# Performance work log

Hardware: AMD Instinct MI355X
Metric: run time of the kernel (lower is better)

Reference implementation:

```python
import jax, jax.numpy as jnp
import numpy as np

N_NODES = 50000
N_EDGES = 600000
D = 128


def setup_inputs() -> dict:
    key = jax.random.key(0)
    k1, k2, k3, k4, k5, k6 = jax.random.split(key, 6)
    x = jax.random.normal(k1, (N_NODES, D), dtype=jnp.float32)
    edge_index = jax.random.randint(k2, (2, N_EDGES), 0, N_NODES, dtype=jnp.int64)
    # nn.Linear default init: U(-1/sqrt(fan_in), 1/sqrt(fan_in))
    bound = 1.0 / np.sqrt(D)
    W1 = jax.random.uniform(k3, (D, D), minval=-bound, maxval=bound, dtype=jnp.float32)
    b1 = jax.random.uniform(k4, (D,), minval=-bound, maxval=bound, dtype=jnp.float32)
    W2 = jax.random.uniform(k5, (D, D), minval=-bound, maxval=bound, dtype=jnp.float32)
    b2 = jax.random.uniform(k6, (D,), minval=-bound, maxval=bound, dtype=jnp.float32)
    return {"x": x, "edge_index": edge_index, "W1": W1, "b1": b1, "W2": W2, "b2": b2}


def reference(x, edge_index, W1, b1, W2, b2):
    row, col = edge_index[0], edge_index[1]
    n = x.shape[0]
    # degree of each node as aggregation target, clamped to >= 1
    deg = jax.ops.segment_sum(jnp.ones(row.shape, dtype=x.dtype), row, num_segments=n)
    deg = jnp.maximum(deg, 1.0)[:, None]  # [N, 1]
    # round 1: gather neighbors, scatter-add by row, normalize, linear+relu
    agg = jax.ops.segment_sum(x[col], row, num_segments=n)  # [N, D]
    h = jax.nn.relu((agg / deg) @ W1.T + b1)
    # round 2
    agg2 = jax.ops.segment_sum(h[col], row, num_segments=n)  # [N, D]
    return jax.nn.relu((agg2 / deg) @ W2.T + b2)
```

## Files before the change

### kernel.cpp

```cpp
#include <hip/hip_runtime.h>
#include <hip/hip_fp16.h>

#define D 128
#define TILE_R 64
#define NC 8

typedef _Float16 h8 __attribute__((ext_vector_type(8)));
typedef float f4 __attribute__((ext_vector_type(4)));

__global__ __launch_bounds__(256) void prep_kernel(int* __restrict__ hist8, int n8,
                                                   const float* __restrict__ W1,
                                                   __half* __restrict__ WB1,
                                                   const float* __restrict__ W2,
                                                   __half* __restrict__ WB2) {
    if (blockIdx.x < 2) {
        const float* W = blockIdx.x ? W2 : W1;
        __half* WB     = blockIdx.x ? WB2 : WB1;
        for (int idx = threadIdx.x; idx < D * D; idx += 256) {
            int j  = idx & 7;
            int l  = (idx >> 3) & 63;
            int kk = (idx >> 9) & 3;
            int c  = idx >> 11;
            int k   = kk * 32 + (l >> 4) * 8 + j;
            int col = c * 16 + (l & 15);
            WB[idx] = __float2half(W[col * D + k]);
        }
        return;
    }
    int i = (blockIdx.x - 2) * 256 + threadIdx.x;
    if (i < n8) hist8[i] = 0;
}

__device__ inline h8 load_frag(const __half* p) { return *(const h8*)p; }
__device__ inline h8 load_frag(const float* p) {
    float4 u = *(const float4*)p;
    float4 v = *(const float4*)(p + 4);
    h8 r;
    r[0] = (_Float16)u.x; r[1] = (_Float16)u.y; r[2] = (_Float16)u.z; r[3] = (_Float16)u.w;
    r[4] = (_Float16)v.x; r[5] = (_Float16)v.y; r[6] = (_Float16)v.z; r[7] = (_Float16)v.w;
    return r;
}

template <typename T>
__device__ inline void linear_coal(const T* __restrict__ src,
                                   const __half* __restrict__ WB,
                                   __half* __restrict__ z, int n, int blk) {
    __shared__ __half Zs[64][132];
    int l    = threadIdx.x & 63;
    int wv   = threadIdx.x >> 6;
    int row0 = blk * TILE_R + wv * 16;
    int arow = row0 + (l & 15);
    bool rowok = arow < n;

    h8 a[4];
#pragma unroll
    for (int kk = 0; kk < 4; ++kk) {
        if (rowok)
            a[kk] = load_frag(&src[(size_t)arow * D + kk * 32 + (l >> 4) * 8]);
        else
            a[kk] = (h8)(_Float16)0.0f;
    }

    int lr0 = wv * 16 + (l >> 4) * 4;
#pragma unroll
    for (int c = 0; c < 8; ++c) {
        f4 acc = {0.f, 0.f, 0.f, 0.f};
#pragma unroll
        for (int kk = 0; kk < 4; ++kk) {
            h8 b = *(const h8*)&WB[(((c * 4 + kk) * 64) + l) * 8];
            acc = __builtin_amdgcn_mfma_f32_16x16x32_f16(a[kk], b, acc, 0, 0, 0);
        }
        int col = c * 16 + (l & 15);
#pragma unroll
        for (int r = 0; r < 4; ++r) Zs[lr0 + r][col] = __float2half(acc[r]);
    }
    __syncthreads();

    int row = threadIdx.x >> 2;
    int cb  = (threadIdx.x & 3) * 32;
    int gro = blk * TILE_R + row;
    if (gro < n) {
        float2 p0 = *(const float2*)&Zs[row][cb];
        float2 p1 = *(const float2*)&Zs[row][cb + 4];
        float2 p2 = *(const float2*)&Zs[row][cb + 8];
        float2 p3 = *(const float2*)&Zs[row][cb + 12];
        float2 p4 = *(const float2*)&Zs[row][cb + 16];
        float2 p5 = *(const float2*)&Zs[row][cb + 20];
        float2 p6 = *(const float2*)&Zs[row][cb + 24];
        float2 p7 = *(const float2*)&Zs[row][cb + 28];
        __half* zp = &z[(size_t)gro * D + cb];
        *(float4*)(zp)      = make_float4(p0.x, p0.y, p1.x, p1.y);
        *(float4*)(zp + 8)  = make_float4(p2.x, p2.y, p3.x, p3.y);
        *(float4*)(zp + 16) = make_float4(p4.x, p4.y, p5.x, p5.y);
        *(float4*)(zp + 24) = make_float4(p6.x, p6.y, p7.x, p7.y);
    }
}

__global__ __launch_bounds__(256) void hist_linear_kernel(const int* __restrict__ ei, int e,
                                                          int* __restrict__ hist8, int nlin,
                                                          const float* __restrict__ x,
                                                          const __half* __restrict__ WB,
                                                          __half* __restrict__ z, int n) {
    if (blockIdx.x >= nlin) {
        int chunk = blockIdx.x - nlin;
        int i = chunk * 256 + threadIdx.x;
        if (i < e) atomicAdd(&hist8[(chunk & (NC - 1)) * n + ei[i]], 1);
        return;
    }
    linear_coal<float>(x, WB, z, n, blockIdx.x);
}

__global__ __launch_bounds__(256) void partial_kernel(const int* __restrict__ hist8,
                                                      int* __restrict__ bsum, int n) {
    int i = blockIdx.x * 256 + threadIdx.x;
    int v = 0;
    if (i < n) {
#pragma unroll
        for (int c = 0; c < NC; ++c) v += hist8[c * n + i];
    }
#pragma unroll
    for (int off = 1; off < 64; off <<= 1) v += __shfl_xor(v, off);
    __shared__ int ws[4];
    int lane = threadIdx.x & 63, w = threadIdx.x >> 6;
    if (lane == 0) ws[w] = v;
    __syncthreads();
    if (threadIdx.x == 0) bsum[blockIdx.x] = ws[0] + ws[1] + ws[2] + ws[3];
}

__global__ __launch_bounds__(256) void finalize_kernel(const int* __restrict__ hist8,
                                                       const int* __restrict__ bsum,
                                                       int* __restrict__ offsets,
                                                       int* __restrict__ deg,
                                                       int* __restrict__ cursor8,
                                                       float* __restrict__ rdeg, int n) {
    __shared__ int wt[4];
    int t = threadIdx.x, lane = t & 63, w = t >> 6;

    int p = 0;
    for (int k = t; k < blockIdx.x; k += 256) p += bsum[k];
#pragma unroll
    for (int off = 1; off < 64; off <<= 1) p += __shfl_xor(p, off);
    if (lane == 0) wt[w] = p;
    __syncthreads();
    int blockbase = wt[0] + wt[1] + wt[2] + wt[3];
    __syncthreads();

    int i = blockIdx.x * 256 + t;
    int cnt[NC];
    int tot = 0;
    if (i < n) {
#pragma unroll
        for (int c = 0; c < NC; ++c) { cnt[c] = hist8[c * n + i]; tot += cnt[c]; }
    } else {
#pragma unroll
        for (int c = 0; c < NC; ++c) cnt[c] = 0;
    }
    int iv = tot;
#pragma unroll
    for (int off = 1; off < 64; off <<= 1) {
        int n2 = __shfl_up(iv, off);
        if (lane >= off) iv += n2;
    }
    if (lane == 63) wt[w] = iv;
    __syncthreads();
    int add = blockbase;
    for (int k = 0; k < w; ++k) add += wt[k];
    int excl = iv - tot + add;
    if (i < n) {
        offsets[i] = excl;
        deg[i]     = tot;
        rdeg[i]    = 1.0f / fmaxf((float)tot, 1.0f);
        int run = excl;
#pragma unroll
        for (int c = 0; c < NC; ++c) { cursor8[c * n + i] = run; run += cnt[c]; }
    }
}

__global__ __launch_bounds__(256) void fill_kernel(const int* __restrict__ ei, int e,
                                                   int* __restrict__ cursor8,
                                                   int* __restrict__ csr, int n) {
    int i = blockIdx.x * 256 + threadIdx.x;
    if (i < e) {
        int r = ei[i];
        int c = ei[e + i];
        int pos = atomicAdd(&cursor8[(blockIdx.x & (NC - 1)) * n + r], 1);
        csr[pos] = c;
    }
}

__device__ inline void addh8(float* a, float4 v) {
    const __half2* h = (const __half2*)&v;
    float2 f0 = __half22float2(h[0]);
    float2 f1 = __half22float2(h[1]);
    float2 f2 = __half22float2(h[2]);
    float2 f3 = __half22float2(h[3]);
    a[0] += f0.x; a[1] += f0.y; a[2] += f1.x; a[3] += f1.y;
    a[4] += f2.x; a[5] += f2.y; a[6] += f3.x; a[7] += f3.y;
}

__device__ inline void gather_core(const float4* __restrict__ base, int start, int cnt,
                                   int gl, const int* __restrict__ csr, float* acc) {
    int i = 0;
    for (; i + 8 <= cnt; i += 8) {
        int c0 = csr[start + i];
        int c1 = csr[start + i + 1];
        int c2 = csr[start + i + 2];
        int c3 = csr[start + i + 3];
        int c4 = csr[start + i + 4];
        int c5 = csr[start + i + 5];
        int c6 = csr[start + i + 6];
        int c7 = csr[start + i + 7];
        float4 v0 = base[(size_t)c0 * 16 + gl];
        float4 v1 = base[(size_t)c1 * 16 + gl];
        float4 v2 = base[(size_t)c2 * 16 + gl];
        float4 v3 = base[(size_t)c3 * 16 + gl];
        float4 v4 = base[(size_t)c4 * 16 + gl];
        float4 v5 = base[(size_t)c5 * 16 + gl];
        float4 v6 = base[(size_t)c6 * 16 + gl];
        float4 v7 = base[(size_t)c7 * 16 + gl];
        addh8(acc, v0); addh8(acc, v1); addh8(acc, v2); addh8(acc, v3);
        addh8(acc, v4); addh8(acc, v5); addh8(acc, v6); addh8(acc, v7);
    }
    if (i + 4 <= cnt) {
        int c0 = csr[start + i];
        int c1 = csr[start + i + 1];
        int c2 = csr[start + i + 2];
        int c3 = csr[start + i + 3];
        float4 v0 = base[(size_t)c0 * 16 + gl];
        float4 v1 = base[(size_t)c1 * 16 + gl];
        float4 v2 = base[(size_t)c2 * 16 + gl];
        float4 v3 = base[(size_t)c3 * 16 + gl];
        addh8(acc, v0); addh8(acc, v1); addh8(acc, v2); addh8(acc, v3);
        i += 4;
    }
    int rem = cnt - i;
    if (rem > 0) {
        int c0 = csr[start + i];
        int c1 = csr[start + min(i + 1, cnt - 1)];
        int c2 = csr[start + min(i + 2, cnt - 1)];
        float4 v0 = base[(size_t)c0 * 16 + gl];
        float4 v1 = base[(size_t)c1 * 16 + gl];
        float4 v2 = base[(size_t)c2 * 16 + gl];
        addh8(acc, v0);
        if (rem > 1) addh8(acc, v1);
        if (rem > 2) addh8(acc, v2);
    }
}

__global__ __launch_bounds__(512) void gather_linear_kernel(const __half* __restrict__ z1,
                                                            const int* __restrict__ offsets,
                                                            const int* __restrict__ deg,
                                                            const int* __restrict__ csr,
                                                            const float* __restrict__ rdeg,
                                                            const float* __restrict__ bias,
                                                            const __half* __restrict__ WB2,
                                                            __half* __restrict__ z2, int n) {
    __shared__ __half Hs[32][136];
    int t    = threadIdx.x;
    int wv   = t >> 6;
    int lane = t & 63;
    int g    = lane >> 4;
    int gl   = lane & 15;
    int lrow = wv * 4 + g;
    int node = blockIdx.x * 32 + lrow;

    if (node < n) {
        float acc[8] = {0.f, 0.f, 0.f, 0.f, 0.f, 0.f, 0.f, 0.f};
        gather_core((const float4*)z1, offsets[node], deg[node], gl, csr, acc);
        float rd = rdeg[node];
        float4 b0 = ((const float4*)bias)[gl * 2];
        float4 b1 = ((const float4*)bias)[gl * 2 + 1];
        __half2 hp[4];
        hp[0] = __float22half2_rn(make_float2(fmaxf(acc[0] * rd + b0.x, 0.f),
                                              fmaxf(acc[1] * rd + b0.y, 0.f)));
        hp[1] = __float22half2_rn(make_float2(fmaxf(acc[2] * rd + b0.z, 0.f),
                                              fmaxf(acc[3] * rd + b0.w, 0.f)));
        hp[2] = __float22half2_rn(make_float2(fmaxf(acc[4] * rd + b1.x, 0.f),
                                              fmaxf(acc[5] * rd + b1.y, 0.f)));
        hp[3] = __float22half2_rn(make_float2(fmaxf(acc[6] * rd + b1.z, 0.f),
                                              fmaxf(acc[7] * rd + b1.w, 0.f)));
        *(float4*)&Hs[lrow][gl * 8] = *(const float4*)hp;
    }
    __syncthreads();

    int r0 = (wv >> 2) * 16;
    int arow = r0 + (lane & 15);
    h8 a[4];
#pragma unroll
    for (int kk = 0; kk < 4; ++kk)
        a[kk] = *(const h8*)&Hs[arow][kk * 32 + (lane >> 4) * 8];

    int srow = blockIdx.x * 32 + r0 + (lane >> 4) * 4;
#pragma unroll
    for (int cc = 0; cc < 2; ++cc) {
        int c = (wv & 3) * 2 + cc;
        f4 acc = {0.f, 0.f, 0.f, 0.f};
#pragma unroll
        for (int kk = 0; kk < 4; ++kk) {
            h8 b = *(const h8*)&WB2[(((c * 4 + kk) * 64) + lane) * 8];
            acc = __builtin_amdgcn_mfma_f32_16x16x32_f16(a[kk], b, acc, 0, 0, 0);
        }
        int col = c * 16 + (lane & 15);
#pragma unroll
        for (int r = 0; r < 4; ++r) {
            int ro = srow + r;
            if (ro < n) z2[(size_t)ro * D + col] = __float2half(acc[r]);
        }
    }
}

__global__ __launch_bounds__(256) void gather_kernel(const __half* __restrict__ z,
                                                     const int* __restrict__ offsets,
                                                     const int* __restrict__ deg,
                                                     const int* __restrict__ csr,
                                                     const float* __restrict__ rdeg,
                                                     const float* __restrict__ bias,
                                                     float* __restrict__ out, int n) {
    int tid  = blockIdx.x * 256 + threadIdx.x;
    int wave = tid >> 6;
    int lane = threadIdx.x & 63;
    int g    = lane >> 4;
    int gl   = lane & 15;
    int node = wave * 4 + g;
    if (node >= n) return;

    float acc[8] = {0.f, 0.f, 0.f, 0.f, 0.f, 0.f, 0.f, 0.f};
    gather_core((const float4*)z, offsets[node], deg[node], gl, csr, acc);

    float rd = rdeg[node];
    float4 b0 = ((const float4*)bias)[gl * 2];
    float4 b1 = ((const float4*)bias)[gl * 2 + 1];
    float4* o4 = (float4*)out;
    o4[(size_t)node * 32 + gl * 2] =
        make_float4(fmaxf(acc[0] * rd + b0.x, 0.f), fmaxf(acc[1] * rd + b0.y, 0.f),
                    fmaxf(acc[2] * rd + b0.z, 0.f), fmaxf(acc[3] * rd + b0.w, 0.f));
    o4[(size_t)node * 32 + gl * 2 + 1] =
        make_float4(fmaxf(acc[4] * rd + b1.x, 0.f), fmaxf(acc[5] * rd + b1.y, 0.f),
                    fmaxf(acc[6] * rd + b1.z, 0.f), fmaxf(acc[7] * rd + b1.w, 0.f));
}

extern "C" void kernel_launch(void* const* d_in, const int* in_sizes, int n_in,
                              void* d_out, int out_size, void* d_ws, size_t ws_size,
                              hipStream_t stream) {
    const float* x  = (const float*)d_in[0];
    const int*   ei = (const int*)d_in[1];
    const float* W1 = (const float*)d_in[2];
    const float* b1 = (const float*)d_in[3];
    const float* W2 = (const float*)d_in[4];
    const float* b2 = (const float*)d_in[5];
    float* out = (float*)d_out;

    int N = in_sizes[0] / D;
    int E = in_sizes[1] / 2;
    int NB = (N + 255) / 256;

    int* hist8   = (int*)d_ws;
    int* cursor8 = hist8 + NC * N;
    int* offsets = cursor8 + NC * N;
    int* deg     = offsets + N;
    int* csr     = deg + N;
    float* rdeg  = (float*)(csr + E);
    int* bsum    = (int*)(rdeg + N);
    __half* WB1  = (__half*)(bsum + ((NB + 3) & ~3));
    __half* WB2  = WB1 + D * D;
    __half* zz   = WB2 + D * D;
    __half* zz2  = zz + (size_t)N * D;

    int NB8   = (NC * N + 255) / 256;
    int nhist = (E + 255) / 256;
    int nblk  = (N + TILE_R - 1) / TILE_R;
    int gfblk = (N + 31) / 32;
    int gblk  = ((N + 3) / 4 * 64 + 255) / 256;

    prep_kernel<<<NB8 + 2, 256, 0, stream>>>(hist8, NC * N, W1, WB1, W2, WB2);
    hist_linear_kernel<<<nblk + nhist, 256, 0, stream>>>(ei, E, hist8, nblk, x, WB1, zz, N);
    partial_kernel<<<NB, 256, 0, stream>>>(hist8, bsum, N);
    finalize_kernel<<<NB, 256, 0, stream>>>(hist8, bsum, offsets, deg, cursor8, rdeg, N);
    fill_kernel<<<nhist, 256, 0, stream>>>(ei, E, cursor8, csr, N);
    gather_linear_kernel<<<gfblk, 512, 0, stream>>>(zz, offsets, deg, csr, rdeg, b1,
                                                    WB2, zz2, N);
    gather_kernel<<<gblk, 256, 0, stream>>>(zz2, offsets, deg, csr, rdeg, b2, out, N);
}
```

Measured before the change: 146.4 us.

## Fuse scan and CSR fill into one persistent kernel with grid barriers

Merges the partial-sum, finalize/scan and fill kernels into a single persistent kernel of 384 blocks that uses atomic-counter grid barriers between phases, removing two kernel launches and their gaps. Fill becomes a grid-stride loop. The number of histogram/cursor copies is also raised from 8 to 16 to spread atomic contention. The cost is more memory for zeroing and scanning the histograms, spin-wait barriers that assume all 384 blocks are co-resident, and a hang risk if they are not.

Measured after the change: 224.8 us. +53.5%, slower.

```diff
diff --git a/kernel.cpp b/kernel.cpp
--- a/kernel.cpp
+++ b/kernel.cpp
@@ -3,12 +3,14 @@
 
 #define D 128
 #define TILE_R 64
-#define NC 8
+#define NC 16
+#define SFB 384
 
 typedef _Float16 h8 __attribute__((ext_vector_type(8)));
 typedef float f4 __attribute__((ext_vector_type(4)));
 
 __global__ __launch_bounds__(256) void prep_kernel(int* __restrict__ hist8, int n8,
+                                                   int* __restrict__ sync,
                                                    const float* __restrict__ W1,
                                                    __half* __restrict__ WB1,
                                                    const float* __restrict__ W2,
@@ -27,6 +29,7 @@
         }
         return;
     }
+    if (blockIdx.x == 2 && threadIdx.x < 8) sync[threadIdx.x] = 0;
     int i = (blockIdx.x - 2) * 256 + threadIdx.x;
     if (i < n8) hist8[i] = 0;
 }
@@ -110,80 +113,92 @@
     linear_coal<float>(x, WB, z, n, blockIdx.x);
 }
 
-__global__ __launch_bounds__(256) void partial_kernel(const int* __restrict__ hist8,
-                                                      int* __restrict__ bsum, int n) {
-    int i = blockIdx.x * 256 + threadIdx.x;
-    int v = 0;
-    if (i < n) {
-#pragma unroll
-        for (int c = 0; c < NC; ++c) v += hist8[c * n + i];
-    }
-#pragma unroll
-    for (int off = 1; off < 64; off <<= 1) v += __shfl_xor(v, off);
-    __shared__ int ws[4];
-    int lane = threadIdx.x & 63, w = threadIdx.x >> 6;
-    if (lane == 0) ws[w] = v;
+__device__ inline void gsync(int* cnt, int target) {
     __syncthreads();
-    if (threadIdx.x == 0) bsum[blockIdx.x] = ws[0] + ws[1] + ws[2] + ws[3];
-}
-
-__global__ __launch_bounds__(256) void finalize_kernel(const int* __restrict__ hist8,
-                                                       const int* __restrict__ bsum,
-                                                       int* __restrict__ offsets,
-                                                       int* __restrict__ deg,
-                                                       int* __restrict__ cursor8,
-                                                       float* __restrict__ rdeg, int n) {
+    if (threadIdx.x == 0) {
+        __threadfence();
+        atomicAdd(cnt, 1);
+        while (atomicAdd(cnt, 0) < target) {}
+        __threadfence();
+    }
+    __syncthreads();
+}
+
+__global__ __launch_bounds__(256) void scan_fill_kernel(const int* __restrict__ ei, int e,
+                                                        int* __restrict__ hist8,
+                                                        int* __restrict__ bsum,
+                                                        int* __restrict__ sync,
+                                                        int* __restrict__ offsets,
+                                                        int* __restrict__ deg,
+                                                        int* __restrict__ cursor8,
+                                                        float* __restrict__ rdeg,
+                                                        int* __restrict__ csr,
+                                                        int n, int nscanb) {
     __shared__ int wt[4];
     int t = threadIdx.x, lane = t & 63, w = t >> 6;
 
-    int p = 0;
-    for (int k = t; k < blockIdx.x; k += 256) p += bsum[k];
-#pragma unroll
-    for (int off = 1; off < 64; off <<= 1) p += __shfl_xor(p, off);
-    if (lane == 0) wt[w] = p;
-    __syncthreads();
-    int blockbase = wt[0] + wt[1] + wt[2] + wt[3];
-    __syncthreads();
-
-    int i = blockIdx.x * 256 + t;
-    int cnt[NC];
-    int tot = 0;
-    if (i < n) {
-#pragma unroll
-        for (int c = 0; c < NC; ++c) { cnt[c] = hist8[c * n + i]; tot += cnt[c]; }
-    } else {
-#pragma unroll
-        for (int c = 0; c < NC; ++c) cnt[c] = 0;
-    }
-    int iv = tot;
-#pragma unroll
-    for (int off = 1; off < 64; off <<= 1) {
-        int n2 = __shfl_up(iv, off);
-        if (lane >= off) iv += n2;
-    }
-    if (lane == 63) wt[w] = iv;
-    __syncthreads();
-    int add = blockbase;
-    for (int k = 0; k < w; ++k) add += wt[k];
-    int excl = iv - tot + add;
-    if (i < n) {
-        offsets[i] = excl;
-        deg[i]     = tot;
-        rdeg[i]    = 1.0f / fmaxf((float)tot, 1.0f);
-        int run = excl;
-#pragma unroll
-        for (int c = 0; c < NC; ++c) { cursor8[c * n + i] = run; run += cnt[c]; }
-    }
-}
-
-__global__ __launch_bounds__(256) void fill_kernel(const int* __restrict__ ei, int e,
-                                                   int* __restrict__ cursor8,
-                                                   int* __restrict__ csr, int n) {
-    int i = blockIdx.x * 256 + threadIdx.x;
-    if (i < e) {
+    if (blockIdx.x < nscanb) {
+        int i = blockIdx.x * 256 + t;
+        int v = 0;
+        if (i < n) {
+#pragma unroll
+            for (int c = 0; c < NC; ++c) v += hist8[c * n + i];
+        }
+#pragma unroll
+        for (int off = 1; off < 64; off <<= 1) v += __shfl_xor(v, off);
+        if (lane == 0) wt[w] = v;
+        __syncthreads();
+        if (t == 0) bsum[blockIdx.x] = wt[0] + wt[1] + wt[2] + wt[3];
+    }
+    gsync(&sync[0], gridDim.x);
+
+    if (blockIdx.x < nscanb) {
+        int p = 0;
+        for (int k = t; k < blockIdx.x; k += 256) p += bsum[k];
+#pragma unroll
+        for (int off = 1; off < 64; off <<= 1) p += __shfl_xor(p, off);
+        __syncthreads();
+        if (lane == 0) wt[w] = p;
+        __syncthreads();
+        int blockbase = wt[0] + wt[1] + wt[2] + wt[3];
+
+        int i = blockIdx.x * 256 + t;
+        int cnt[NC];
+        int tot = 0;
+        if (i < n) {
+#pragma unroll
+            for (int c = 0; c < NC; ++c) { cnt[c] = hist8[c * n + i]; tot += cnt[c]; }
+        } else {
+#pragma unroll
+            for (int c = 0; c < NC; ++c) cnt[c] = 0;
+        }
+        int iv = tot;
+#pragma unroll
+        for (int off = 1; off < 64; off <<= 1) {
+            int n2 = __shfl_up(iv, off);
+            if (lane >= off) iv += n2;
+        }
+        __syncthreads();
+        if (lane == 63) wt[w] = iv;
+        __syncthreads();
+        int add = blockbase;
+        for (int k = 0; k < w; ++k) add += wt[k];
+        int excl = iv - tot + add;
+        if (i < n) {
+            offsets[i] = excl;
+            deg[i]     = tot;
+            rdeg[i]    = 1.0f / fmaxf((float)tot, 1.0f);
+            int run = excl;
+#pragma unroll
+            for (int c = 0; c < NC; ++c) { cursor8[c * n + i] = run; run += cnt[c]; }
+        }
+    }
+    gsync(&sync[1], gridDim.x);
+
+    for (int i = blockIdx.x * 256 + t; i < e; i += gridDim.x * 256) {
         int r = ei[i];
         int c = ei[e + i];
-        int pos = atomicAdd(&cursor8[(blockIdx.x & (NC - 1)) * n + r], 1);
+        int pos = atomicAdd(&cursor8[((i >> 8) & (NC - 1)) * n + r], 1);
         csr[pos] = c;
     }
 }
@@ -361,22 +376,22 @@
     int* csr     = deg + N;
     float* rdeg  = (float*)(csr + E);
     int* bsum    = (int*)(rdeg + N);
-    __half* WB1  = (__half*)(bsum + ((NB + 3) & ~3));
+    int* sync    = bsum + ((NB + 3) & ~3);
+    __half* WB1  = (__half*)(sync + 8);
     __half* WB2  = WB1 + D * D;
     __half* zz   = WB2 + D * D;
     __half* zz2  = zz + (size_t)N * D;
 
-    int NB8   = (NC * N + 255) / 256;
+    int NZ    = (NC * N + 255) / 256;
     int nhist = (E + 255) / 256;
     int nblk  = (N + TILE_R - 1) / TILE_R;
     int gfblk = (N + 31) / 32;
     int gblk  = ((N + 3) / 4 * 64 + 255) / 256;
 
-    prep_kernel<<<NB8 + 2, 256, 0, stream>>>(hist8, NC * N, W1, WB1, W2, WB2);
+    prep_kernel<<<NZ + 2, 256, 0, stream>>>(hist8, NC * N, sync, W1, WB1, W2, WB2);
     hist_linear_kernel<<<nblk + nhist, 256, 0, stream>>>(ei, E, hist8, nblk, x, WB1, zz, N);
-    partial_kernel<<<NB, 256, 0, stream>>>(hist8, bsum, N);
-    finalize_kernel<<<NB, 256, 0, stream>>>(hist8, bsum, offsets, deg, cursor8, rdeg, N);
-    fill_kernel<<<nhist, 256, 0, stream>>>(ei, E, cursor8, csr, N);
+    scan_fill_kernel<<<SFB, 256, 0, stream>>>(ei, E, hist8, bsum, sync, offsets, deg,
+                                              cursor8, rdeg, csr, N, NB);
     gather_linear_kernel<<<gfblk, 512, 0, stream>>>(zz, offsets, deg, csr, rdeg, b1,
                                                     WB2, zz2, N);
     gather_kernel<<<gblk, 256, 0, stream>>>(zz2, offsets, deg, csr, rdeg, b2, out, N);
```
